# Performance work log

Hardware: AMD Instinct MI355X
Metric: run time of the kernel (lower is better)

## Reference

```python
import jax, jax.numpy as jnp
import numpy as np
import math

DIM = 2048
N_HEADS = 16
N_KV_HEADS = 8
HEAD_DIM = DIM // N_HEADS  # 128
N_REP = N_HEADS // N_KV_HEADS  # 2
BLOCK = 128
TOPK = 8
NEG_INF = -10000.0
SEQ = 4096
BS = 1


def _rope_tables(seq_len, head_dim, base=10000.0):
    inv_freq = 1.0 / (base ** (jnp.arange(0, head_dim, 2, dtype=jnp.float32) / head_dim))
    ang = jnp.arange(seq_len, dtype=jnp.float32)[:, None] * inv_freq[None, :]  # [S, hd/2]
    return jnp.cos(ang), jnp.sin(ang)


def _apply_rope(t, cos, sin):
    # t: [bs, S, h, hd]; interleaved pairs
    t1 = t[..., 0::2]
    t2 = t[..., 1::2]
    c = cos[None, :, None, :]
    s = sin[None, :, None, :]
    out_even = t1 * c - t2 * s
    out_odd = t1 * s + t2 * c
    out = jnp.stack([out_even, out_odd], axis=-1)  # [bs,S,h,hd/2,2]
    return out.reshape(t.shape)


def setup_inputs() -> dict:
    key = jax.random.key(0)
    ks = jax.random.split(key, 5)
    scale = 1.0 / math.sqrt(DIM)
    x = jax.random.normal(ks[0], (BS, SEQ, DIM), dtype=jnp.float32)
    wq = jax.random.normal(ks[1], (DIM, N_HEADS * HEAD_DIM), dtype=jnp.float32) * scale
    wk = jax.random.normal(ks[2], (DIM, N_KV_HEADS * HEAD_DIM), dtype=jnp.float32) * scale
    wv = jax.random.normal(ks[3], (DIM, N_KV_HEADS * HEAD_DIM), dtype=jnp.float32) * scale
    wo = jax.random.normal(ks[4], (DIM, DIM), dtype=jnp.float32) * scale
    return {"x": x, "wq": wq, "wk": wk, "wv": wv, "wo": wo}


def reference(x, wq, wk, wv, wo):
    bs, S, _ = x.shape
    inv_sqrt_d = 1.0 / math.sqrt(HEAD_DIM)

    q = (x @ wq).reshape(bs, S, N_HEADS, HEAD_DIM)
    k = (x @ wk).reshape(bs, S, N_KV_HEADS, HEAD_DIM)
    v = (x @ wv).reshape(bs, S, N_KV_HEADS, HEAD_DIM)

    cos, sin = _rope_tables(S, HEAD_DIM)
    q = _apply_rope(q, cos, sin)
    k = _apply_rope(k, cos, sin)

    # [bs, h, S, hd]
    q = jnp.transpose(q, (0, 2, 1, 3))
    k = jnp.transpose(k, (0, 2, 1, 3))
    v = jnp.transpose(v, (0, 2, 1, 3))

    # GQA expand (repeat_interleave over head dim)
    k_e = jnp.repeat(k, N_REP, axis=1)
    v_e = jnp.repeat(v, N_REP, axis=1)

    num_blocks = S // BLOCK  # 32, divides evenly (pad_len == 0)
    k_blocks = k_e.reshape(bs, N_HEADS, num_blocks, BLOCK, HEAD_DIM)
    block_means = k_blocks.mean(axis=3)  # [bs,h,nb,hd]

    gating = jnp.einsum('bhsd,bhnd->bhsn', q, block_means) * inv_sqrt_d
    q_block_idx = jnp.arange(S) // BLOCK
    future_block = q_block_idx[:, None] < jnp.arange(num_blocks)[None, :]  # [S, nb]
    gating = jnp.where(future_block[None, None], NEG_INF, gating)

    curr_k = min(TOPK, num_blocks)
    _, sel_idx = jax.lax.top_k(gating, curr_k)  # [bs,h,S,k]
    selected = jnp.sum(jax.nn.one_hot(sel_idx, num_blocks, dtype=jnp.float32), axis=-2) > 0  # [bs,h,S,nb]

    token_keep = jnp.repeat(selected, BLOCK, axis=-1)[..., :S]  # [bs,h,S,S]
    token_mask = jnp.where(token_keep, 0.0, NEG_INF)

    scores = jnp.einsum('bhsd,bhtd->bhst', q, k_e) * inv_sqrt_d
    causal = jnp.triu(jnp.ones((S, S), dtype=jnp.float32), k=1)  # 1 where future token
    # faithful to source: elementwise max of token mask and causal*neg_inf
    final_mask = jnp.maximum(token_mask, causal[None, None] * NEG_INF)
    scores = scores + final_mask

    probs = jax.nn.softmax(scores.astype(jnp.float32), axis=-1).astype(scores.dtype)
    out = jnp.einsum('bhst,bhtd->bhsd', probs, v_e)
    out = jnp.transpose(out, (0, 2, 1, 3)).reshape(bs, S, N_HEADS * HEAD_DIM)
    return out @ wo
```

## Files before the change

### kernel.cpp

```cpp
#include <hip/hip_runtime.h>
#include <hip/hip_fp16.h>

#define SQ   4096
#define DIMM 2048
#define QKVN 4096

typedef unsigned short u16;
typedef unsigned int u32;
typedef __attribute__((ext_vector_type(8))) short    short8;
typedef __attribute__((ext_vector_type(8))) _Float16 half8;
typedef __attribute__((ext_vector_type(4))) float    f32x4;

__device__ __forceinline__ u16 f2bf(float f) {
  u32 u = __float_as_uint(f);
  u32 r = u + 0x7fffu + ((u >> 16) & 1u);
  return (u16)(r >> 16);
}
__device__ __forceinline__ float bf2f(u16 h) { return __uint_as_float(((u32)h) << 16); }
__device__ __forceinline__ u16 f2h(float f) { return __half_as_ushort(__float2half(f)); }

__device__ __forceinline__ void gll16(const void* g, void* l) {
  __builtin_amdgcn_global_load_lds((const __attribute__((address_space(1))) void*)g,
                                   (__attribute__((address_space(3))) void*)l, 16, 0, 0);
}

__device__ __host__ __forceinline__ int cidx(int qb) {
  return qb < 8 ? qb : qb < 16 ? 8 + (qb - 8) * 2 : qb < 24 ? 24 + (qb - 16) * 3 : 48 + (qb - 24) * 4;
}

__global__ __launch_bounds__(256) void k_tables(float* __restrict__ cosb, float* __restrict__ sinb) {
  int idx = blockIdx.x * 256 + threadIdx.x;
  int pos = idx >> 6, i = idx & 63;
  double f = 1.0 / pow(10000.0, (double)i / 64.0);
  float inv = (float)f;
  float ang = (float)pos * inv;
  cosb[idx] = (float)cos((double)ang);
  sinb[idx] = (float)sin((double)ang);
}

__global__ __launch_bounds__(256) void k_split_x(const float* __restrict__ x,
                                                 u16* __restrict__ xh, u16* __restrict__ xl) {
  size_t base = ((size_t)blockIdx.x * 256 + threadIdx.x) * 4;
  float4 v = *(const float4*)(x + base);
  float vv[4] = {v.x, v.y, v.z, v.w};
  u16 hh[4], ll[4];
#pragma unroll
  for (int j = 0; j < 4; j++) {
    hh[j] = f2bf(vv[j]);
    ll[j] = f2bf(vv[j] - bf2f(hh[j]));
  }
  *(uint2*)(xh + base) = make_uint2((u32)hh[0] | ((u32)hh[1] << 16), (u32)hh[2] | ((u32)hh[3] << 16));
  *(uint2*)(xl + base) = make_uint2((u32)ll[0] | ((u32)ll[1] << 16), (u32)ll[2] | ((u32)ll[3] << 16));
}

__global__ __launch_bounds__(256) void k_trans_split(const float* __restrict__ src, int N,
                                                     u16* __restrict__ dh, u16* __restrict__ dl,
                                                     int rowOff) {
  __shared__ float t[64][65];
  int n0 = blockIdx.x * 64, k0 = blockIdx.y * 64;
  int tid = threadIdx.x;
  int c = tid & 63, r4 = tid >> 6;
#pragma unroll
  for (int it = 0; it < 16; it++) {
    int kk = it * 4 + r4;
    t[kk][c] = src[(size_t)(k0 + kk) * N + n0 + c];
  }
  __syncthreads();
#pragma unroll
  for (int it = 0; it < 16; it++) {
    int nn = it * 4 + r4;
    float v = t[c][nn];
    u16 hh = f2bf(v);
    size_t o = (size_t)(rowOff + n0 + nn) * 2048 + k0 + c;
    dh[o] = hh;
    dl[o] = f2bf(v - bf2f(hh));
  }
}

__global__ __launch_bounds__(256) void k_trans_f16(const float* __restrict__ src, int N,
                                                   u16* __restrict__ dst) {
  __shared__ float t[64][65];
  int n0 = blockIdx.x * 64, k0 = blockIdx.y * 64;
  int tid = threadIdx.x;
  int c = tid & 63, r4 = tid >> 6;
#pragma unroll
  for (int it = 0; it < 16; it++) {
    int kk = it * 4 + r4;
    t[kk][c] = src[(size_t)(k0 + kk) * N + n0 + c];
  }
  __syncthreads();
#pragma unroll
  for (int it = 0; it < 16; it++) {
    int nn = it * 4 + r4;
    dst[(size_t)(n0 + nn) * 2048 + k0 + c] = f2h(t[c][nn]);
  }
}

__global__ __launch_bounds__(256) void k_gemm_qkv(
    const u16* __restrict__ xh, const u16* __restrict__ xl,
    const u16* __restrict__ wth, const u16* __restrict__ wtl,
    float* __restrict__ qkv) {
  __shared__ u16 lds[4 * 128 * 64];
  const int tid = threadIdx.x;
  const int lane = tid & 63, wid = tid >> 6;
  const int rg = lane >> 4, c16 = lane & 15;
  const int m0 = blockIdx.y * 128, n0 = blockIdx.x * 128;
  const int wm = wid >> 1, wn = wid & 1;
  const u16* gsrc = (wid == 0) ? xh + (size_t)m0 * 2048
                  : (wid == 1) ? xl + (size_t)m0 * 2048
                  : (wid == 2) ? wth + (size_t)n0 * 2048
                               : wtl + (size_t)n0 * 2048;
  u16* ldsm = lds + wid * 8192;
  const int sr = lane >> 3, scn = lane & 7;

  f32x4 acc[4][4];
#pragma unroll
  for (int a = 0; a < 4; a++)
#pragma unroll
    for (int b = 0; b < 4; b++) acc[a][b] = (f32x4){0.f, 0.f, 0.f, 0.f};

  for (int k0 = 0; k0 < 2048; k0 += 64) {
#pragma unroll
    for (int i = 0; i < 16; i++) {
      int r = i * 8 + sr;
      int cs = (scn ^ (r & 7)) * 8;
      gll16(gsrc + (size_t)r * 2048 + k0 + cs, ldsm + i * 512);
    }
    __syncthreads();
#pragma unroll
    for (int kk = 0; kk < 2; kk++) {
      short8 ah[4], al[4], bh[4], bl[4];
      int ch = kk * 4 + rg;
#pragma unroll
      for (int mf = 0; mf < 4; mf++) {
        int m = wm * 64 + mf * 16 + c16;
        int off = m * 64 + ((ch ^ (m & 7)) * 8);
        ah[mf] = *(const short8*)(lds + off);
        al[mf] = *(const short8*)(lds + 8192 + off);
      }
#pragma unroll
      for (int nf = 0; nf < 4; nf++) {
        int n = wn * 64 + nf * 16 + c16;
        int off = n * 64 + ((ch ^ (n & 7)) * 8);
        bh[nf] = *(const short8*)(lds + 16384 + off);
        bl[nf] = *(const short8*)(lds + 24576 + off);
      }
#pragma unroll
      for (int mf = 0; mf < 4; mf++)
#pragma unroll
        for (int nf = 0; nf < 4; nf++) {
          acc[mf][nf] = __builtin_amdgcn_mfma_f32_16x16x32_bf16(ah[mf], bh[nf], acc[mf][nf], 0, 0, 0);
          acc[mf][nf] = __builtin_amdgcn_mfma_f32_16x16x32_bf16(ah[mf], bl[nf], acc[mf][nf], 0, 0, 0);
          acc[mf][nf] = __builtin_amdgcn_mfma_f32_16x16x32_bf16(al[mf], bh[nf], acc[mf][nf], 0, 0, 0);
        }
    }
    __syncthreads();
  }
#pragma unroll
  for (int mf = 0; mf < 4; mf++)
#pragma unroll
    for (int nf = 0; nf < 4; nf++)
#pragma unroll
      for (int j = 0; j < 4; j++) {
        int m = m0 + wm * 64 + mf * 16 + rg * 4 + j;
        int n = n0 + wn * 64 + nf * 16 + c16;
        qkv[(size_t)m * QKVN + n] = acc[mf][nf][j];
      }
}

__global__ __launch_bounds__(256) void k_rope_qk(const float* __restrict__ qkv,
                                                 const float* __restrict__ cosb,
                                                 const float* __restrict__ sinb,
                                                 u16* __restrict__ qf, u16* __restrict__ kf2) {
  int idx = blockIdx.x * 256 + threadIdx.x;
  int i = idx & 63;
  int th = idx >> 6;
  int h = th % 24, t = th / 24;
  int c0 = (h < 16) ? h * 128 + 2 * i : 2048 + (h - 16) * 128 + 2 * i;
  float2 eo = *(const float2*)(qkv + (size_t)t * QKVN + c0);
  float c = cosb[t * 64 + i], s = sinb[t * 64 + i];
  float re = eo.x * c - eo.y * s;
  float ro = eo.x * s + eo.y * c;
  if (h < 16) {
    const float QSC = (float)(1.4426950408889634 * 0.08838834764831843);
    u32 pk = (u32)f2h(re * QSC) | ((u32)f2h(ro * QSC) << 16);
    *(u32*)(qf + ((size_t)h * SQ + t) * 128 + 2 * i) = pk;
  } else {
    int hk = h - 16;
    int d = 2 * i;
    int tile = t >> 6, tok = t & 63;
    int kk = tok >> 5, t5 = tok & 31;
    int hf = (t5 >> 2) & 1, c16v = ((t5 >> 3) << 2) | (t5 & 3);
    int dk = d >> 5, rg = (d >> 3) & 3, e = d & 7;
    int lane = rg * 16 + c16v, f = (kk * 2 + hf) * 4 + dk;
    u32 pk = (u32)f2h(re) | ((u32)f2h(ro) << 16);
    *(u32*)(kf2 + ((size_t)((hk * 64 + tile) * 16 + f) * 64 + lane) * 8 + e) = pk;
  }
}

__global__ __launch_bounds__(64) void k_bm(const float* __restrict__ qkv,
                                           const float* __restrict__ cosb,
                                           const float* __restrict__ sinb,
                                           float* __restrict__ bm) {
  int hk = blockIdx.x >> 5, n = blockIdx.x & 31;
  int i = threadIdx.x;
  double se = 0.0, so = 0.0;
  for (int t = 0; t < 128; t++) {
    int tt = n * 128 + t;
    float2 eo = *(const float2*)(qkv + (size_t)tt * QKVN + 2048 + hk * 128 + 2 * i);
    float c = cosb[tt * 64 + i], s = sinb[tt * 64 + i];
    se += (double)(eo.x * c - eo.y * s);
    so += (double)(eo.x * s + eo.y * c);
  }
  float* o = bm + ((size_t)(hk * 32 + n)) * 128 + 2 * i;
  o[0] = (float)(se * (1.0 / 128.0));
  o[1] = (float)(so * (1.0 / 128.0));
}

__global__ __launch_bounds__(64) void k_gate(const float* __restrict__ qkv,
                                             const float* __restrict__ cosb,
                                             const float* __restrict__ sinb,
                                             const float* __restrict__ bm,
                                             unsigned char* __restrict__ sel) {
  __shared__ float q[64][129];
  __shared__ float bml[32 * 128];
  int bz = blockIdx.x;
  int h = bz / 48;
  int rem = bz % 48;
  int b = 8 + (rem >> 1);
  int half = rem & 1;
  int tid = threadIdx.x;
  int hk = h >> 1;
  for (int rr = 0; rr < 64; rr++) {
    int ss = b * 128 + half * 64 + rr;
    float2 eo = *(const float2*)(qkv + (size_t)ss * QKVN + h * 128 + 2 * tid);
    float c = cosb[ss * 64 + tid], sn = sinb[ss * 64 + tid];
    q[rr][2 * tid]     = eo.x * c - eo.y * sn;
    q[rr][2 * tid + 1] = eo.x * sn + eo.y * c;
  }
  for (int o = tid; o < (b + 1) * 128; o += 64) bml[o] = bm[(size_t)hk * 32 * 128 + o];
  __syncthreads();
  int s = b * 128 + half * 64 + tid;
  double gb = 0.0;
  for (int d = 0; d < 128; d++) gb += (double)q[tid][d] * (double)bml[b * 128 + d];
  int cnt = 0;
  for (int n = 0; n < b; n++) {
    double g = 0.0;
    for (int d = 0; d < 128; d++) g += (double)q[tid][d] * (double)bml[n * 128 + d];
    cnt += (g >= gb) ? 1 : 0;
  }
  sel[h * SQ + s] = (cnt <= 7) ? 1 : 0;
}

__global__ __launch_bounds__(256) void k_vt2(const float* __restrict__ qkv, u16* __restrict__ vt2) {
  int hk = blockIdx.x & 7, tile = blockIdx.x >> 3;
  int tid = threadIdx.x;
  u16* dst = vt2 + (size_t)(hk * 64 + tile) * 8192;
#pragma unroll
  for (int rep = 0; rep < 16; rep++) {
    int idx = rep * 256 + tid;
    int tp = idx >> 7;
    int d  = idx & 127;
    int t  = tile * 64 + tp * 2;
    float v0 = qkv[(size_t)t * QKVN + 3072 + hk * 128 + d];
    float v1 = qkv[(size_t)(t + 1) * QKVN + 3072 + hk * 128 + d];
    int tok = tp * 2;
    int kk = tok >> 5, rg = (tok >> 3) & 3, e = tok & 7;
    int nf = d >> 4, c16v = d & 15;
    int lane = rg * 16 + c16v, g = kk * 8 + nf;
    u32 pk = (u32)f2h(v0) | ((u32)f2h(v1) << 16);
    *(u32*)(dst + ((size_t)(g * 64 + lane)) * 8 + e) = pk;
  }
}

__global__ __launch_bounds__(256) void k_attn_chunk(
    const u16* __restrict__ qf, const u16* __restrict__ kf2, const u16* __restrict__ vt2,
    const unsigned char* __restrict__ sel, float* __restrict__ po, float* __restrict__ ml) {
  __shared__ u16 lds[2][16384];
  const int L = blockIdx.x;
  const int hk = L & 7;
  const int c = L >> 3;
  const int h = hk * 2 + (c & 1);
  const int cc = c >> 1;
  int qb, chunk;
  if (cc < 8)       { qb = cc;                   chunk = 0; }
  else if (cc < 24) { qb = 8 + ((cc - 8) >> 1);  chunk = (cc - 8) & 1; }
  else if (cc < 48) { qb = 16 + (cc - 24) / 3;   chunk = (cc - 24) % 3; }
  else              { qb = 24 + ((cc - 48) >> 2); chunk = (cc - 48) & 3; }
  const int nt128 = (qb < 8) ? 8 : (qb + 1);
  const int t0 = chunk * 16;
  const int t1 = (t0 + 16 < nt128 * 2) ? t0 + 16 : nt128 * 2;
  const int tid = threadIdx.x;
  const int lane = tid & 63, wid = tid >> 6;
  const int rg = lane >> 4, c16 = lane & 15;
  const bool hasMask = (qb >= 8);

  half8 aq[2][4];
#pragma unroll
  for (int mi = 0; mi < 2; mi++)
#pragma unroll
    for (int dk = 0; dk < 4; dk++) {
      int srow = qb * 128 + wid * 32 + mi * 16 + c16;
      aq[mi][dk] = *(const half8*)(qf + ((size_t)h * SQ + srow) * 128 + dk * 32 + rg * 8);
    }

  bool os2[2] = {true, true};
  if (hasMask) {
#pragma unroll
    for (int mi = 0; mi < 2; mi++)
      os2[mi] = sel[h * SQ + qb * 128 + wid * 32 + mi * 16 + c16] != 0;
  }

  f32x4 accO[2][8];
#pragma unroll
  for (int mi = 0; mi < 2; mi++)
#pragma unroll
    for (int nf = 0; nf < 8; nf++) accO[mi][nf] = (f32x4){0.f, 0.f, 0.f, 0.f};
  float mrun[2] = {-1e30f, -1e30f}, lrun[2] = {0.f, 0.f};

  const u16* kbase = kf2 + (size_t)hk * 64 * 8192;
  const u16* vbase = vt2 + (size_t)hk * 64 * 8192;

  auto stage = [&](int b, int n) {
    const u16* ks = kbase + (size_t)n * 8192;
    const u16* vs = vbase + (size_t)n * 8192;
#pragma unroll
    for (int r = 0; r < 4; r++)
      gll16(ks + r * 2048 + wid * 512 + lane * 8, &lds[b][r * 2048 + wid * 512]);
#pragma unroll
    for (int r = 0; r < 4; r++)
      gll16(vs + r * 2048 + wid * 512 + lane * 8, &lds[b][8192 + r * 2048 + wid * 512]);
  };

  stage(0, t0);

  for (int n = t0; n < t1; n++) {
    const int cur = (n - t0) & 1;
    __syncthreads();
    if (n + 1 < t1) stage(cur ^ 1, n + 1);
    const u16* lb = &lds[cur][0];

    f32x4 st[2][2][2];
#pragma unroll
    for (int kk = 0; kk < 2; kk++)
#pragma unroll
      for (int hf = 0; hf < 2; hf++)
#pragma unroll
        for (int mi = 0; mi < 2; mi++) st[kk][hf][mi] = (f32x4){0.f, 0.f, 0.f, 0.f};

    __builtin_amdgcn_s_setprio(1);
#pragma unroll
    for (int kk = 0; kk < 2; kk++)
#pragma unroll
      for (int hf = 0; hf < 2; hf++) {
        half8 ka[4];
#pragma unroll
        for (int dk = 0; dk < 4; dk++)
          ka[dk] = *(const half8*)(lb + ((kk * 2 + hf) * 4 + dk) * 512 + lane * 8);
#pragma unroll
        for (int dk = 0; dk < 4; dk++) {
          st[kk][hf][0] = __builtin_amdgcn_mfma_f32_16x16x32_f16(ka[dk], aq[0][dk], st[kk][hf][0], 0, 0, 0);
          st[kk][hf][1] = __builtin_amdgcn_mfma_f32_16x16x32_f16(ka[dk], aq[1][dk], st[kk][hf][1], 0, 0, 0);
        }
      }
    __builtin_amdgcn_s_setprio(0);

    if (hasMask && n >= 2 * qb) {
#pragma unroll
      for (int mi = 0; mi < 2; mi++) {
        if (!os2[mi]) {
          int row = qb * 128 + wid * 32 + mi * 16 + c16;
#pragma unroll
          for (int kk = 0; kk < 2; kk++)
#pragma unroll
            for (int hf = 0; hf < 2; hf++)
#pragma unroll
              for (int j = 0; j < 4; j++) {
                int tg = n * 64 + kk * 32 + rg * 8 + hf * 4 + j;
                if (tg > row) st[kk][hf][mi][j] = -1e30f;
              }
        }
      }
    }

#pragma unroll
    for (int mi = 0; mi < 2; mi++) {
      float mt = st[0][0][mi][0];
#pragma unroll
      for (int kk = 0; kk < 2; kk++)
#pragma unroll
        for (int hf = 0; hf < 2; hf++)
#pragma unroll
          for (int j = 0; j < 4; j++)
            if (kk | hf | j) mt = fmaxf(mt, st[kk][hf][mi][j]);
      mt = fmaxf(mt, __shfl_xor(mt, 16, 64));
      mt = fmaxf(mt, __shfl_xor(mt, 32, 64));
      if (!__all(mt <= mrun[mi] + 8.f)) {
        float mnew = fmaxf(mrun[mi], mt);
        float sc = exp2f(mrun[mi] - mnew);
        mrun[mi] = mnew;
        lrun[mi] *= sc;
#pragma unroll
        for (int nf = 0; nf < 8; nf++) accO[mi][nf] *= sc;
      }
      float ps = 0.f;
#pragma unroll
      for (int kk = 0; kk < 2; kk++)
#pragma unroll
        for (int hf = 0; hf < 2; hf++)
#pragma unroll
          for (int j = 0; j < 4; j++) {
            float p = exp2f(st[kk][hf][mi][j] - mrun[mi]);
            st[kk][hf][mi][j] = p;
            ps += p;
          }
      ps += __shfl_xor(ps, 16, 64);
      ps += __shfl_xor(ps, 32, 64);
      lrun[mi] += ps;
    }

    half8 pa[2][2];
#pragma unroll
    for (int kk = 0; kk < 2; kk++)
#pragma unroll
      for (int mi = 0; mi < 2; mi++) {
        union { half8 v; _Float16 e[8]; } pu;
#pragma unroll
        for (int hf = 0; hf < 2; hf++)
#pragma unroll
          for (int j = 0; j < 4; j++)
            pu.e[hf * 4 + j] = (_Float16)st[kk][hf][mi][j];
        pa[kk][mi] = pu.v;
      }

    __builtin_amdgcn_s_setprio(1);
#pragma unroll
    for (int kk = 0; kk < 2; kk++)
#pragma unroll
      for (int nf = 0; nf < 8; nf++) {
        half8 va = *(const half8*)(lb + 8192 + (kk * 8 + nf) * 512 + lane * 8);
        accO[0][nf] = __builtin_amdgcn_mfma_f32_16x16x32_f16(va, pa[kk][0], accO[0][nf], 0, 0, 0);
        accO[1][nf] = __builtin_amdgcn_mfma_f32_16x16x32_f16(va, pa[kk][1], accO[1][nf], 0, 0, 0);
      }
    __builtin_amdgcn_s_setprio(0);
  }

  const int pidx = h * 80 + cidx(qb) + chunk;
  float* pob = po + (size_t)pidx * 16384;
#pragma unroll
  for (int mi = 0; mi < 2; mi++) {
    int row = wid * 32 + mi * 16 + c16;
#pragma unroll
    for (int nf = 0; nf < 8; nf++)
      *(f32x4*)&pob[row * 128 + nf * 16 + rg * 4] = accO[mi][nf];
  }
  if (rg == 0) {
#pragma unroll
    for (int mi = 0; mi < 2; mi++) {
      int row = wid * 32 + mi * 16 + c16;
      ml[(size_t)pidx * 256 + row * 2]     = mrun[mi];
      ml[(size_t)pidx * 256 + row * 2 + 1] = lrun[mi];
    }
  }
}

__global__ __launch_bounds__(256) void k_attn_combine(
    const float* __restrict__ po, const float* __restrict__ ml, u16* __restrict__ attn) {
  const int qb = blockIdx.x, h = blockIdx.y;
  const int nc = (qb < 8) ? 1 : (qb < 16) ? 2 : (qb < 24) ? 3 : 4;
  const int base = h * 80 + cidx(qb);
  const int tid = threadIdx.x;
  const int r = tid >> 1, h64 = (tid & 1) * 64;
  float m[4], l[4], M = -1e30f;
#pragma unroll
  for (int ci = 0; ci < 4; ci++) {
    if (ci < nc) {
      m[ci] = ml[(size_t)(base + ci) * 256 + r * 2];
      l[ci] = ml[(size_t)(base + ci) * 256 + r * 2 + 1];
    } else { m[ci] = -1e30f; l[ci] = 0.f; }
    M = fmaxf(M, m[ci]);
  }
  float w[4], Ls = 0.f;
#pragma unroll
  for (int ci = 0; ci < 4; ci++) { w[ci] = exp2f(m[ci] - M); Ls += w[ci] * l[ci]; }
  float inv = 1.0f / Ls;
  for (int d = 0; d < 64; d += 4) {
    float4 a = make_float4(0.f, 0.f, 0.f, 0.f);
#pragma unroll
    for (int ci = 0; ci < 4; ci++) {
      if (ci < nc) {
        const float4 v = *(const float4*)&po[(size_t)(base + ci) * 16384 + r * 128 + h64 + d];
        a.x += w[ci] * v.x; a.y += w[ci] * v.y; a.z += w[ci] * v.z; a.w += w[ci] * v.w;
      }
    }
    u32 p0 = (u32)f2h(a.x * inv) | ((u32)f2h(a.y * inv) << 16);
    u32 p1 = (u32)f2h(a.z * inv) | ((u32)f2h(a.w * inv) << 16);
    *(uint2*)&attn[(size_t)(qb * 128 + r) * DIMM + h * 128 + h64 + d] = make_uint2(p0, p1);
  }
}

__global__ __launch_bounds__(256) void k_gemm_out(
    const u16* __restrict__ attn, const u16* __restrict__ wot, float* __restrict__ out) {
  __shared__ u16 lds[2 * 128 * 64];
  const int tid = threadIdx.x;
  const int lane = tid & 63, wid = tid >> 6;
  const int rg = lane >> 4, c16 = lane & 15;
  const int m0 = blockIdx.y * 128, n0 = blockIdx.x * 128;
  const int wm = wid >> 1, wn = wid & 1;
  const u16* gsrc = (wid < 2) ? attn + (size_t)m0 * 2048 : wot + (size_t)n0 * 2048;
  const int sr = lane >> 3, scn = lane & 7;

  f32x4 acc[4][4];
#pragma unroll
  for (int a = 0; a < 4; a++)
#pragma unroll
    for (int b = 0; b < 4; b++) acc[a][b] = (f32x4){0.f, 0.f, 0.f, 0.f};

  for (int k0 = 0; k0 < 2048; k0 += 64) {
#pragma unroll
    for (int i = 0; i < 8; i++) {
      int slot = wid * 8 + i;
      int s2 = slot & 15;
      int r = s2 * 8 + sr;
      int cs = (scn ^ (r & 7)) * 8;
      gll16(gsrc + (size_t)r * 2048 + k0 + cs, lds + slot * 512);
    }
    __syncthreads();
#pragma unroll
    for (int kk = 0; kk < 2; kk++) {
      half8 a[4], b[4];
      int ch = kk * 4 + rg;
#pragma unroll
      for (int mf = 0; mf < 4; mf++) {
        int m = wm * 64 + mf * 16 + c16;
        a[mf] = *(const half8*)(lds + m * 64 + ((ch ^ (m & 7)) * 8));
      }
#pragma unroll
      for (int nf = 0; nf < 4; nf++) {
        int n = wn * 64 + nf * 16 + c16;
        b[nf] = *(const half8*)(lds + 8192 + n * 64 + ((ch ^ (n & 7)) * 8));
      }
#pragma unroll
      for (int mf = 0; mf < 4; mf++)
#pragma unroll
        for (int nf = 0; nf < 4; nf++)
          acc[mf][nf] = __builtin_amdgcn_mfma_f32_16x16x32_f16(a[mf], b[nf], acc[mf][nf], 0, 0, 0);
    }
    __syncthreads();
  }
#pragma unroll
  for (int mf = 0; mf < 4; mf++)
#pragma unroll
    for (int nf = 0; nf < 4; nf++)
#pragma unroll
      for (int j = 0; j < 4; j++) {
        int m = m0 + wm * 64 + mf * 16 + rg * 4 + j;
        int n = n0 + wn * 64 + nf * 16 + c16;
        out[(size_t)m * DIMM + n] = acc[mf][nf][j];
      }
}

extern "C" void kernel_launch(void* const* d_in, const int* in_sizes, int n_in,
                              void* d_out, int out_size, void* d_ws, size_t ws_size,
                              hipStream_t stream) {
  (void)in_sizes; (void)n_in; (void)out_size; (void)ws_size;
  const float* x  = (const float*)d_in[0];
  const float* wq = (const float*)d_in[1];
  const float* wk = (const float*)d_in[2];
  const float* wv = (const float*)d_in[3];
  const float* wo = (const float*)d_in[4];
  float* out = (float*)d_out;

  char* ws = (char*)d_ws;
  const size_t MB = 1024 * 1024;
  char* A = ws;
  u16*   xh  = (u16*)(A);
  u16*   xl  = (u16*)(A + 16 * MB);
  u16*   wth = (u16*)(A + 32 * MB);
  u16*   wtl = (u16*)(A + 48 * MB);
  float* qkv = (float*)(A + 64 * MB);
  float* po  = (float*)(A);
  float* ml  = (float*)(A + 88 * MB);
  char* B = ws + 128 * MB;
  size_t off = 0;
  auto alloc = [&](size_t b) { char* p = B + off; off += (b + 255) & ~(size_t)255; return p; };
  u16*   wot  = (u16*)alloc((size_t)DIMM * DIMM * 2);
  float* cosb = (float*)alloc((size_t)SQ * 64 * 4);
  float* sinb = (float*)alloc((size_t)SQ * 64 * 4);
  u16*   qf   = (u16*)alloc((size_t)16 * SQ * 128 * 2);
  u16*   kf2  = (u16*)alloc((size_t)8 * SQ * 128 * 2);
  u16*   vt2  = (u16*)alloc((size_t)8 * 128 * SQ * 2);
  float* bm   = (float*)alloc((size_t)8 * 32 * 128 * 4);
  unsigned char* sel = (unsigned char*)alloc((size_t)16 * SQ);
  u16*   attn = (u16*)alloc((size_t)SQ * DIMM * 2);

  k_tables<<<SQ * 64 / 256, 256, 0, stream>>>(cosb, sinb);
  k_split_x<<<(SQ * DIMM) / (256 * 4), 256, 0, stream>>>(x, xh, xl);
  k_trans_split<<<dim3(32, 32), 256, 0, stream>>>(wq, 2048, wth, wtl, 0);
  k_trans_split<<<dim3(16, 32), 256, 0, stream>>>(wk, 1024, wth, wtl, 2048);
  k_trans_split<<<dim3(16, 32), 256, 0, stream>>>(wv, 1024, wth, wtl, 3072);
  k_trans_f16<<<dim3(32, 32), 256, 0, stream>>>(wo, 2048, wot);
  k_gemm_qkv<<<dim3(32, 32), 256, 0, stream>>>(xh, xl, wth, wtl, qkv);
  k_rope_qk<<<(SQ * 24 * 64) / 256, 256, 0, stream>>>(qkv, cosb, sinb, qf, kf2);
  k_vt2<<<512, 256, 0, stream>>>(qkv, vt2);
  k_bm<<<256, 64, 0, stream>>>(qkv, cosb, sinb, bm);
  k_gate<<<16 * 48, 64, 0, stream>>>(qkv, cosb, sinb, bm, sel);
  k_attn_chunk<<<1280, 256, 0, stream>>>(qf, kf2, vt2, sel, po, ml);
  k_attn_combine<<<dim3(32, 16), 256, 0, stream>>>(po, ml, attn);
  k_gemm_out<<<dim3(16, 32), 256, 0, stream>>>(attn, wot, out);
}
```

Baseline: 612.9 us.

## Shrink attention KV tile, store fp16 normalized partials, swizzle GEMM block order

The attention chunk kernel now processes 32-key tiles instead of 64, which halves LDS use and keeps the same per-chunk key range through doubled iteration counts. Each chunk normalizes its partial output and writes it as fp16, along with a single log-sum-exp value per row. The combine kernel is simplified to match, which cuts the partial-output write and read traffic. The QKV and output GEMMs remap block indices with an XCD-style swizzle to improve L2 locality. The trade-offs are more loop iterations with smaller MFMA batches, and extra fp16 rounding in the partials.

```diff
diff --git a/kernel.cpp b/kernel.cpp
--- a/kernel.cpp
+++ b/kernel.cpp
@@ -18,6 +18,7 @@
 }
 __device__ __forceinline__ float bf2f(u16 h) { return __uint_as_float(((u32)h) << 16); }
 __device__ __forceinline__ u16 f2h(float f) { return __half_as_ushort(__float2half(f)); }
+__device__ __forceinline__ float h2f(u16 h) { union { u16 u; _Float16 f; } c; c.u = h; return (float)c.f; }
 
 __device__ __forceinline__ void gll16(const void* g, void* l) {
   __builtin_amdgcn_global_load_lds((const __attribute__((address_space(1))) void*)g,
@@ -104,7 +105,9 @@
   const int tid = threadIdx.x;
   const int lane = tid & 63, wid = tid >> 6;
   const int rg = lane >> 4, c16 = lane & 15;
-  const int m0 = blockIdx.y * 128, n0 = blockIdx.x * 128;
+  const int bid0 = blockIdx.y * 32 + blockIdx.x;
+  const int swz = (bid0 & 7) * 128 + (bid0 >> 3);
+  const int m0 = (swz >> 5) * 128, n0 = (swz & 31) * 128;
   const int wm = wid >> 1, wn = wid & 1;
   const u16* gsrc = (wid == 0) ? xh + (size_t)m0 * 2048
                   : (wid == 1) ? xl + (size_t)m0 * 2048
@@ -275,8 +278,8 @@
 
 __global__ __launch_bounds__(256) void k_attn_chunk(
     const u16* __restrict__ qf, const u16* __restrict__ kf2, const u16* __restrict__ vt2,
-    const unsigned char* __restrict__ sel, float* __restrict__ po, float* __restrict__ ml) {
-  __shared__ u16 lds[2][16384];
+    const unsigned char* __restrict__ sel, u16* __restrict__ po, float* __restrict__ ml) {
+  __shared__ u16 lds[2][8192];
   const int L = blockIdx.x;
   const int hk = L & 7;
   const int c = L >> 3;
@@ -288,8 +291,8 @@
   else if (cc < 48) { qb = 16 + (cc - 24) / 3;   chunk = (cc - 24) % 3; }
   else              { qb = 24 + ((cc - 48) >> 2); chunk = (cc - 48) & 3; }
   const int nt128 = (qb < 8) ? 8 : (qb + 1);
-  const int t0 = chunk * 16;
-  const int t1 = (t0 + 16 < nt128 * 2) ? t0 + 16 : nt128 * 2;
+  const int t0 = chunk * 32;
+  const int t1 = (t0 + 32 < nt128 * 4) ? t0 + 32 : nt128 * 4;
   const int tid = threadIdx.x;
   const int lane = tid & 63, wid = tid >> 6;
   const int rg = lane >> 4, c16 = lane & 15;
@@ -322,14 +325,13 @@
   const u16* vbase = vt2 + (size_t)hk * 64 * 8192;
 
   auto stage = [&](int b, int n) {
-    const u16* ks = kbase + (size_t)n * 8192;
-    const u16* vs = vbase + (size_t)n * 8192;
-#pragma unroll
-    for (int r = 0; r < 4; r++)
+    const u16* ks = kbase + (size_t)n * 4096;
+    const u16* vs = vbase + (size_t)n * 4096;
+#pragma unroll
+    for (int r = 0; r < 2; r++) {
       gll16(ks + r * 2048 + wid * 512 + lane * 8, &lds[b][r * 2048 + wid * 512]);
-#pragma unroll
-    for (int r = 0; r < 4; r++)
-      gll16(vs + r * 2048 + wid * 512 + lane * 8, &lds[b][8192 + r * 2048 + wid * 512]);
+      gll16(vs + r * 2048 + wid * 512 + lane * 8, &lds[b][4096 + r * 2048 + wid * 512]);
+    }
   };
 
   stage(0, t0);
@@ -340,59 +342,51 @@
     if (n + 1 < t1) stage(cur ^ 1, n + 1);
     const u16* lb = &lds[cur][0];
 
-    f32x4 st[2][2][2];
-#pragma unroll
-    for (int kk = 0; kk < 2; kk++)
-#pragma unroll
-      for (int hf = 0; hf < 2; hf++)
-#pragma unroll
-        for (int mi = 0; mi < 2; mi++) st[kk][hf][mi] = (f32x4){0.f, 0.f, 0.f, 0.f};
+    f32x4 st[2][2];
+#pragma unroll
+    for (int hf = 0; hf < 2; hf++)
+#pragma unroll
+      for (int mi = 0; mi < 2; mi++) st[hf][mi] = (f32x4){0.f, 0.f, 0.f, 0.f};
 
     __builtin_amdgcn_s_setprio(1);
 #pragma unroll
-    for (int kk = 0; kk < 2; kk++)
-#pragma unroll
-      for (int hf = 0; hf < 2; hf++) {
-        half8 ka[4];
-#pragma unroll
-        for (int dk = 0; dk < 4; dk++)
-          ka[dk] = *(const half8*)(lb + ((kk * 2 + hf) * 4 + dk) * 512 + lane * 8);
-#pragma unroll
-        for (int dk = 0; dk < 4; dk++) {
-          st[kk][hf][0] = __builtin_amdgcn_mfma_f32_16x16x32_f16(ka[dk], aq[0][dk], st[kk][hf][0], 0, 0, 0);
-          st[kk][hf][1] = __builtin_amdgcn_mfma_f32_16x16x32_f16(ka[dk], aq[1][dk], st[kk][hf][1], 0, 0, 0);
-        }
-      }
+    for (int hf = 0; hf < 2; hf++) {
+      half8 ka[4];
+#pragma unroll
+      for (int dk = 0; dk < 4; dk++)
+        ka[dk] = *(const half8*)(lb + (hf * 4 + dk) * 512 + lane * 8);
+#pragma unroll
+      for (int dk = 0; dk < 4; dk++) {
+        st[hf][0] = __builtin_amdgcn_mfma_f32_16x16x32_f16(ka[dk], aq[0][dk], st[hf][0], 0, 0, 0);
+        st[hf][1] = __builtin_amdgcn_mfma_f32_16x16x32_f16(ka[dk], aq[1][dk], st[hf][1], 0, 0, 0);
+      }
+    }
     __builtin_amdgcn_s_setprio(0);
 
-    if (hasMask && n >= 2 * qb) {
+    if (hasMask && n >= 4 * qb) {
 #pragma unroll
       for (int mi = 0; mi < 2; mi++) {
         if (!os2[mi]) {
           int row = qb * 128 + wid * 32 + mi * 16 + c16;
 #pragma unroll
-          for (int kk = 0; kk < 2; kk++)
-#pragma unroll
-            for (int hf = 0; hf < 2; hf++)
-#pragma unroll
-              for (int j = 0; j < 4; j++) {
-                int tg = n * 64 + kk * 32 + rg * 8 + hf * 4 + j;
-                if (tg > row) st[kk][hf][mi][j] = -1e30f;
-              }
+          for (int hf = 0; hf < 2; hf++)
+#pragma unroll
+            for (int j = 0; j < 4; j++) {
+              int tg = n * 32 + rg * 8 + hf * 4 + j;
+              if (tg > row) st[hf][mi][j] = -1e30f;
+            }
         }
       }
     }
 
 #pragma unroll
     for (int mi = 0; mi < 2; mi++) {
-      float mt = st[0][0][mi][0];
-#pragma unroll
-      for (int kk = 0; kk < 2; kk++)
-#pragma unroll
-        for (int hf = 0; hf < 2; hf++)
-#pragma unroll
-          for (int j = 0; j < 4; j++)
-            if (kk | hf | j) mt = fmaxf(mt, st[kk][hf][mi][j]);
+      float mt = st[0][mi][0];
+#pragma unroll
+      for (int hf = 0; hf < 2; hf++)
+#pragma unroll
+        for (int j = 0; j < 4; j++)
+          if (hf | j) mt = fmaxf(mt, st[hf][mi][j]);
       mt = fmaxf(mt, __shfl_xor(mt, 16, 64));
       mt = fmaxf(mt, __shfl_xor(mt, 32, 64));
       if (!__all(mt <= mrun[mi] + 8.f)) {
@@ -405,96 +399,88 @@
       }
       float ps = 0.f;
 #pragma unroll
-      for (int kk = 0; kk < 2; kk++)
-#pragma unroll
-        for (int hf = 0; hf < 2; hf++)
-#pragma unroll
-          for (int j = 0; j < 4; j++) {
-            float p = exp2f(st[kk][hf][mi][j] - mrun[mi]);
-            st[kk][hf][mi][j] = p;
-            ps += p;
-          }
+      for (int hf = 0; hf < 2; hf++)
+#pragma unroll
+        for (int j = 0; j < 4; j++) {
+          float p = exp2f(st[hf][mi][j] - mrun[mi]);
+          st[hf][mi][j] = p;
+          ps += p;
+        }
       ps += __shfl_xor(ps, 16, 64);
       ps += __shfl_xor(ps, 32, 64);
       lrun[mi] += ps;
     }
 
-    half8 pa[2][2];
-#pragma unroll
-    for (int kk = 0; kk < 2; kk++)
-#pragma unroll
-      for (int mi = 0; mi < 2; mi++) {
-        union { half8 v; _Float16 e[8]; } pu;
-#pragma unroll
-        for (int hf = 0; hf < 2; hf++)
-#pragma unroll
-          for (int j = 0; j < 4; j++)
-            pu.e[hf * 4 + j] = (_Float16)st[kk][hf][mi][j];
-        pa[kk][mi] = pu.v;
-      }
+    half8 pa[2];
+#pragma unroll
+    for (int mi = 0; mi < 2; mi++) {
+      union { half8 v; _Float16 e[8]; } pu;
+#pragma unroll
+      for (int hf = 0; hf < 2; hf++)
+#pragma unroll
+        for (int j = 0; j < 4; j++)
+          pu.e[hf * 4 + j] = (_Float16)st[hf][mi][j];
+      pa[mi] = pu.v;
+    }
 
     __builtin_amdgcn_s_setprio(1);
 #pragma unroll
-    for (int kk = 0; kk < 2; kk++)
-#pragma unroll
-      for (int nf = 0; nf < 8; nf++) {
-        half8 va = *(const half8*)(lb + 8192 + (kk * 8 + nf) * 512 + lane * 8);
-        accO[0][nf] = __builtin_amdgcn_mfma_f32_16x16x32_f16(va, pa[kk][0], accO[0][nf], 0, 0, 0);
-        accO[1][nf] = __builtin_amdgcn_mfma_f32_16x16x32_f16(va, pa[kk][1], accO[1][nf], 0, 0, 0);
-      }
+    for (int nf = 0; nf < 8; nf++) {
+      half8 va = *(const half8*)(lb + 4096 + nf * 512 + lane * 8);
+      accO[0][nf] = __builtin_amdgcn_mfma_f32_16x16x32_f16(va, pa[0], accO[0][nf], 0, 0, 0);
+      accO[1][nf] = __builtin_amdgcn_mfma_f32_16x16x32_f16(va, pa[1], accO[1][nf], 0, 0, 0);
+    }
     __builtin_amdgcn_s_setprio(0);
   }
 
   const int pidx = h * 80 + cidx(qb) + chunk;
-  float* pob = po + (size_t)pidx * 16384;
+  u16* pob = po + (size_t)pidx * 16384;
 #pragma unroll
   for (int mi = 0; mi < 2; mi++) {
+    float inv = 1.0f / lrun[mi];
     int row = wid * 32 + mi * 16 + c16;
 #pragma unroll
-    for (int nf = 0; nf < 8; nf++)
-      *(f32x4*)&pob[row * 128 + nf * 16 + rg * 4] = accO[mi][nf];
-  }
-  if (rg == 0) {
-#pragma unroll
-    for (int mi = 0; mi < 2; mi++) {
-      int row = wid * 32 + mi * 16 + c16;
-      ml[(size_t)pidx * 256 + row * 2]     = mrun[mi];
-      ml[(size_t)pidx * 256 + row * 2 + 1] = lrun[mi];
-    }
+    for (int nf = 0; nf < 8; nf++) {
+      u32 p0 = (u32)f2h(accO[mi][nf][0] * inv) | ((u32)f2h(accO[mi][nf][1] * inv) << 16);
+      u32 p1 = (u32)f2h(accO[mi][nf][2] * inv) | ((u32)f2h(accO[mi][nf][3] * inv) << 16);
+      *(uint2*)&pob[row * 128 + nf * 16 + rg * 4] = make_uint2(p0, p1);
+    }
+    if (rg == 0)
+      ml[(size_t)pidx * 128 + row] = mrun[mi] + log2f(lrun[mi]);
   }
 }
 
 __global__ __launch_bounds__(256) void k_attn_combine(
-    const float* __restrict__ po, const float* __restrict__ ml, u16* __restrict__ attn) {
+    const u16* __restrict__ po, const float* __restrict__ ml, u16* __restrict__ attn) {
   const int qb = blockIdx.x, h = blockIdx.y;
   const int nc = (qb < 8) ? 1 : (qb < 16) ? 2 : (qb < 24) ? 3 : 4;
   const int base = h * 80 + cidx(qb);
   const int tid = threadIdx.x;
   const int r = tid >> 1, h64 = (tid & 1) * 64;
-  float m[4], l[4], M = -1e30f;
+  float mp[4], M = -1e30f;
 #pragma unroll
   for (int ci = 0; ci < 4; ci++) {
-    if (ci < nc) {
-      m[ci] = ml[(size_t)(base + ci) * 256 + r * 2];
-      l[ci] = ml[(size_t)(base + ci) * 256 + r * 2 + 1];
-    } else { m[ci] = -1e30f; l[ci] = 0.f; }
-    M = fmaxf(M, m[ci]);
-  }
-  float w[4], Ls = 0.f;
-#pragma unroll
-  for (int ci = 0; ci < 4; ci++) { w[ci] = exp2f(m[ci] - M); Ls += w[ci] * l[ci]; }
-  float inv = 1.0f / Ls;
+    mp[ci] = (ci < nc) ? ml[(size_t)(base + ci) * 128 + r] : -1e30f;
+    M = fmaxf(M, mp[ci]);
+  }
+  float w[4], Ws = 0.f;
+#pragma unroll
+  for (int ci = 0; ci < 4; ci++) { w[ci] = exp2f(mp[ci] - M); Ws += (ci < nc) ? w[ci] : 0.f; }
+  float inv = 1.0f / Ws;
   for (int d = 0; d < 64; d += 4) {
-    float4 a = make_float4(0.f, 0.f, 0.f, 0.f);
+    float a[4] = {0.f, 0.f, 0.f, 0.f};
 #pragma unroll
     for (int ci = 0; ci < 4; ci++) {
       if (ci < nc) {
-        const float4 v = *(const float4*)&po[(size_t)(base + ci) * 16384 + r * 128 + h64 + d];
-        a.x += w[ci] * v.x; a.y += w[ci] * v.y; a.z += w[ci] * v.z; a.w += w[ci] * v.w;
-      }
-    }
-    u32 p0 = (u32)f2h(a.x * inv) | ((u32)f2h(a.y * inv) << 16);
-    u32 p1 = (u32)f2h(a.z * inv) | ((u32)f2h(a.w * inv) << 16);
+        uint2 u = *(const uint2*)&po[(size_t)(base + ci) * 16384 + r * 128 + h64 + d];
+        a[0] += w[ci] * h2f((u16)(u.x & 0xffff));
+        a[1] += w[ci] * h2f((u16)(u.x >> 16));
+        a[2] += w[ci] * h2f((u16)(u.y & 0xffff));
+        a[3] += w[ci] * h2f((u16)(u.y >> 16));
+      }
+    }
+    u32 p0 = (u32)f2h(a[0] * inv) | ((u32)f2h(a[1] * inv) << 16);
+    u32 p1 = (u32)f2h(a[2] * inv) | ((u32)f2h(a[3] * inv) << 16);
     *(uint2*)&attn[(size_t)(qb * 128 + r) * DIMM + h * 128 + h64 + d] = make_uint2(p0, p1);
   }
 }
@@ -505,7 +491,9 @@
   const int tid = threadIdx.x;
   const int lane = tid & 63, wid = tid >> 6;
   const int rg = lane >> 4, c16 = lane & 15;
-  const int m0 = blockIdx.y * 128, n0 = blockIdx.x * 128;
+  const int bid0 = blockIdx.y * 16 + blockIdx.x;
+  const int swz = (bid0 & 7) * 64 + (bid0 >> 3);
+  const int m0 = (swz >> 4) * 128, n0 = (swz & 15) * 128;
   const int wm = wid >> 1, wn = wid & 1;
   const u16* gsrc = (wid < 2) ? attn + (size_t)m0 * 2048 : wot + (size_t)n0 * 2048;
   const int sr = lane >> 3, scn = lane & 7;
@@ -579,8 +567,8 @@
   u16*   wth = (u16*)(A + 32 * MB);
   u16*   wtl = (u16*)(A + 48 * MB);
   float* qkv = (float*)(A + 64 * MB);
-  float* po  = (float*)(A);
-  float* ml  = (float*)(A + 88 * MB);
+  u16*   po  = (u16*)(A);
+  float* ml  = (float*)(A + 48 * MB);
   char* B = ws + 128 * MB;
   size_t off = 0;
   auto alloc = [&](size_t b) { char* p = B + off; off += (b + 255) & ~(size_t)255; return p; };
```

New measurement: 568.6 us. 1.08x faster.
